# Kernel tuning notes

Measured on AMD Instinct MI355X. Metric: run time of the kernel, lower is better.

## Reference

```python
import jax, jax.numpy as jnp
import numpy as np

N = 100000      # nodes
E = 1600000     # edges (avg degree 16)
F_IN = 128      # num_features
H = 64          # num_hidden
C = 40          # num_classes


def setup_inputs() -> dict:
    key = jax.random.key(0)
    ks = jax.random.split(key, 12)
    glorot = lambda k, fi, fo: jax.random.normal(k, (fi, fo), jnp.float32) * np.float32(1.0 / np.sqrt(fi))
    return {
        "x": jax.random.normal(ks[0], (N, F_IN), jnp.float32),
        "edge_index": jax.random.randint(ks[1], (2, E), 0, N, jnp.int64),
        "conv0_w": glorot(ks[2], F_IN, H), "conv0_b": jnp.zeros((H,), jnp.float32),
        "lin0_w": glorot(ks[3], H, H),     "lin0_b": jnp.zeros((H,), jnp.float32),
        "conv1_w": glorot(ks[4], H, H),    "conv1_b": jnp.zeros((H,), jnp.float32),
        "lin1_w": glorot(ks[5], H, H),     "lin1_b": jnp.zeros((H,), jnp.float32),
        "out_w": glorot(ks[6], 2 * H, C),  "out_b": jnp.zeros((C,), jnp.float32),
    }


def _gcn_conv(h, W, b, src, dst, norm, n):
    # h: [N, din] -> transform then symmetric-normalized scatter-add aggregation
    m = (h @ W)[src] * norm[:, None]           # [E+N, dout] gathered messages
    return jax.ops.segment_sum(m, dst, num_segments=n) + b


def reference(x, edge_index, conv0_w, conv0_b, lin0_w, lin0_b,
              conv1_w, conv1_b, lin1_w, lin1_b, out_w, out_b):
    n = x.shape[0]
    loops = jnp.arange(n, dtype=edge_index.dtype)
    src = jnp.concatenate([edge_index[0], loops])  # self-loops appended (GCNConv default)
    dst = jnp.concatenate([edge_index[1], loops])
    deg = jax.ops.segment_sum(jnp.ones_like(dst, x.dtype), dst, num_segments=n)
    dinv = jnp.where(deg > 0, jax.lax.rsqrt(deg), 0.0)
    norm = dinv[src] * dinv[dst]                   # D^-1/2 A D^-1/2 edge weights

    # layer 0 (dropout omitted: eval mode for deterministic reference)
    h = jax.nn.elu(_gcn_conv(x, conv0_w, conv0_b, src, dst, norm, n))
    y0 = h @ lin0_w + lin0_b
    # layer 1
    h = jax.nn.elu(_gcn_conv(h, conv1_w, conv1_b, src, dst, norm, n))
    y1 = h @ lin1_w + lin1_b

    z = jnp.concatenate([y0, y1], axis=1)          # [N, 2H] jumping-knowledge concat
    return z @ out_w + out_b                       # [N, C]
```

## Files before the change

kernel.cpp:

```cpp
#include <hip/hip_runtime.h>

#define DEVFN __device__ __forceinline__

typedef __attribute__((ext_vector_type(8))) short short8;
typedef __attribute__((ext_vector_type(4))) float float4v;

DEVFN float bf2f(unsigned short u) {
    union { unsigned int i; float f; } c;
    c.i = ((unsigned int)u) << 16;
    return c.f;
}

DEVFN unsigned short f2bf(float f) {
    union { float f; unsigned int i; } c;
    c.f = f;
    unsigned int u = c.i;
    return (unsigned short)((u + 0x7FFFu + ((u >> 16) & 1u)) >> 16);
}

DEVFN void addu4(float* acc, uint4 u) {
    unsigned int w[4] = {u.x, u.y, u.z, u.w};
#pragma unroll
    for (int k = 0; k < 4; k++) {
        union { unsigned int i; float f; } lo, hi;
        lo.i = w[k] << 16;
        hi.i = w[k] & 0xFFFF0000u;
        acc[2 * k]     += lo.f;
        acc[2 * k + 1] += hi.f;
    }
}


#define CHUNK 4096

__global__ __launch_bounds__(256) void k_count(const int* __restrict__ dst,
                                               int* __restrict__ Cmat, int E) {
    __shared__ int lh[1024];
    int t = threadIdx.x;
    for (int b = t; b < 1024; b += 256) lh[b] = 0;
    __syncthreads();
    int i0 = blockIdx.x * CHUNK;
    int i1 = i0 + CHUNK; if (i1 > E) i1 = E;
    for (int i = i0 + t; i < i1; i += 256) atomicAdd(&lh[dst[i] >> 8], 1);
    __syncthreads();
    int* row = Cmat + (size_t)blockIdx.x * 1024;
    for (int b = t; b < 1024; b += 256) row[b] = lh[b];
}

__global__ __launch_bounds__(256) void k_wscan(const int* __restrict__ Cmat,
                                               int* __restrict__ Omat,
                                               int* __restrict__ btot, int gC) {
    int b = (blockIdx.x * 256 + threadIdx.x) >> 6;
    int lane = threadIdx.x & 63;
    int base = 0;
    for (int c0 = 0; c0 < gC; c0 += 64) {
        int c = c0 + lane;
        int x = (c < gC) ? Cmat[(size_t)c * 1024 + b] : 0;
        int orig = x;
#pragma unroll
        for (int off = 1; off < 64; off <<= 1) {
            int y = __shfl_up(x, off);
            if (lane >= off) x += y;
        }
        if (c < gC) Omat[(size_t)c * 1024 + b] = base + x - orig;
        base += __shfl(x, 63);
    }
    if (lane == 0) btot[b] = base;
}

__global__ __launch_bounds__(1024) void k_bscan(const int* __restrict__ btot,
                                                int* __restrict__ boff) {
    __shared__ int s[1024];
    int t = threadIdx.x;
    int v = btot[t];
    s[t] = v;
    __syncthreads();
    for (int o = 1; o < 1024; o <<= 1) {
        int x = (t >= o) ? s[t - o] : 0;
        __syncthreads();
        s[t] += x;
        __syncthreads();
    }
    boff[t] = s[t] - v;
    if (t == 1023) boff[1024] = s[t];
}

__global__ __launch_bounds__(256) void k_part2(const int* __restrict__ src,
                                               const int* __restrict__ dst,
                                               const int* __restrict__ Omat,
                                               const int* __restrict__ boff,
                                               unsigned int* __restrict__ part, int E) {
    __shared__ int lb[1024];
    __shared__ int lc[1024];
    int t = threadIdx.x;
    const int* orow = Omat + (size_t)blockIdx.x * 1024;
    for (int b = t; b < 1024; b += 256) {
        lb[b] = boff[b] + orow[b];
        lc[b] = 0;
    }
    __syncthreads();
    int i0 = blockIdx.x * CHUNK;
    int i1 = i0 + CHUNK; if (i1 > E) i1 = E;
    for (int i = i0 + t; i < i1; i += 256) {
        int d = dst[i];
        int b = d >> 8;
        int r = atomicAdd(&lc[b], 1);
        part[lb[b] + r] = (unsigned int)src[i] | ((unsigned int)(d & 255) << 24);
    }
}

__global__ __launch_bounds__(256) void k_fill_local(const unsigned int* __restrict__ part,
                                                    const int* __restrict__ boff,
                                                    float* __restrict__ dinv,
                                                    int* __restrict__ roff,
                                                    int* __restrict__ csr, int n) {
    __shared__ int lcnt[256];
    __shared__ int lsc[256];
    __shared__ int lcur[256];
    int b = blockIdx.x, t = threadIdx.x;
    int s0 = boff[b], s1 = boff[b + 1];
    lcnt[t] = 0;
    __syncthreads();
    for (int i = s0 + t; i < s1; i += 256) atomicAdd(&lcnt[part[i] >> 24], 1);
    __syncthreads();
    int v = lcnt[t];
    lsc[t] = v;
    __syncthreads();
    for (int o = 1; o < 256; o <<= 1) {
        int x = (t >= o) ? lsc[t - o] : 0;
        __syncthreads();
        lsc[t] += x;
        __syncthreads();
    }
    int excl = lsc[t] - v;
    int node = (b << 8) + t;
    if (node < n) {
        dinv[node] = rsqrtf((float)(v + 1));
        roff[node] = s0 + excl + v;
    }
    lcur[t] = s0 + excl;
    __syncthreads();
    for (int i = s0 + t; i < s1; i += 256) {
        unsigned int p = part[i];
        int pos = atomicAdd(&lcur[p >> 24], 1);
        csr[pos] = (int)(p & 0xFFFFFFu);
    }
}

__global__ void k_fuse(const float* __restrict__ lin0_w, const float* __restrict__ lin0_b,
                       const float* __restrict__ lin1_w, const float* __restrict__ lin1_b,
                       const float* __restrict__ out_w, const float* __restrict__ out_b,
                       float* __restrict__ Wf0, float* __restrict__ Wf1, float* __restrict__ bf) {
    int idx = blockIdx.x * blockDim.x + threadIdx.x;
    if (idx < 2560) {
        int i = idx / 40, j = idx % 40;
        float a = 0.f;
        for (int k = 0; k < 64; k++) a += lin0_w[i * 64 + k] * out_w[k * 40 + j];
        Wf0[idx] = a;
    } else if (idx < 5120) {
        int r = idx - 2560;
        int i = r / 40, j = r % 40;
        float a = 0.f;
        for (int k = 0; k < 64; k++) a += lin1_w[i * 64 + k] * out_w[(64 + k) * 40 + j];
        Wf1[r] = a;
    } else if (idx < 5160) {
        int j = idx - 5120;
        float a = out_b[j];
        for (int k = 0; k < 64; k++) {
            a += lin0_b[k] * out_w[k * 40 + j];
            a += lin1_b[k] * out_w[(64 + k) * 40 + j];
        }
        bf[j] = a;
    }
}

__global__ __launch_bounds__(256) void k_prepw(const float* __restrict__ W0,
                                               const float* __restrict__ W1,
                                               const float* __restrict__ Wf0,
                                               const float* __restrict__ Wf1,
                                               unsigned short* __restrict__ Wb0,
                                               unsigned short* __restrict__ Wb1,
                                               unsigned short* __restrict__ Wfb0,
                                               unsigned short* __restrict__ Wfb1) {
    int tid = blockIdx.x * 256 + threadIdx.x;
    if (tid < 1024) {
        int ks = tid >> 8, rem = tid & 255;
        int nt = rem >> 6, lane = rem & 63;
        int quad = lane >> 4, c = lane & 15;
        union { unsigned short h[8]; uint4 u; } p;
#pragma unroll
        for (int j = 0; j < 8; j++)
            p.h[j] = f2bf(W0[(ks * 32 + quad * 8 + j) * 64 + nt * 16 + c]);
        *(uint4*)(Wb0 + (size_t)tid * 8) = p.u;
    } else if (tid < 1536) {
        int t2 = tid - 1024;
        int ks = t2 >> 8, rem = t2 & 255;
        int nt = rem >> 6, lane = rem & 63;
        int quad = lane >> 4, c = lane & 15;
        union { unsigned short h[8]; uint4 u; } p;
#pragma unroll
        for (int j = 0; j < 8; j++)
            p.h[j] = f2bf(W1[(ks * 32 + quad * 8 + j) * 64 + nt * 16 + c]);
        *(uint4*)(Wb1 + (size_t)t2 * 8) = p.u;
    } else if (tid < 1920) {
        int t2 = tid - 1536;
        int ks = t2 / 192;
        int rem = t2 % 192;
        int nt = rem >> 6, lane = rem & 63;
        int quad = lane >> 4, c = lane & 15;
        int col = nt * 16 + c;
        union { unsigned short h[8]; uint4 u; } p;
#pragma unroll
        for (int j = 0; j < 8; j++)
            p.h[j] = (col < 40) ? f2bf(Wf0[(ks * 32 + quad * 8 + j) * 40 + col]) : (unsigned short)0;
        *(uint4*)(Wfb0 + ((size_t)(ks * 3 + nt) * 64 + lane) * 8) = p.u;
    } else if (tid < 2304) {
        int t2 = tid - 1920;
        int ks = t2 / 192;
        int rem = t2 % 192;
        int nt = rem >> 6, lane = rem & 63;
        int quad = lane >> 4, c = lane & 15;
        int col = nt * 16 + c;
        union { unsigned short h[8]; uint4 u; } p;
#pragma unroll
        for (int j = 0; j < 8; j++)
            p.h[j] = (col < 40) ? f2bf(Wf1[(ks * 32 + quad * 8 + j) * 40 + col]) : (unsigned short)0;
        *(uint4*)(Wfb1 + ((size_t)(ks * 3 + nt) * 64 + lane) * 8) = p.u;
    }
}


__global__ __launch_bounds__(256) void k_gemm_128(const float* __restrict__ A,
                                                  const unsigned short* __restrict__ Wb,
                                                  const float* __restrict__ dinv,
                                                  unsigned short* __restrict__ Cb, int n) {
    __shared__ unsigned short aLDS[64 * 144];
    int t = threadIdx.x;
    int r0 = blockIdx.x * 64;
    for (int idx = t; idx < 2048; idx += 256) {
        int r = idx >> 5;
        int k = (idx & 31) << 2;
        int gr = r0 + r; if (gr >= n) gr = n - 1;
        float4 u = *(const float4*)(A + (size_t)gr * 128 + k);
        int tile = r >> 4, m = r & 15;
        int ks = k >> 5, quad = (k >> 3) & 3, j0 = k & 7;
        int g = (tile * 4 + ks) * 4 + quad;
        union { unsigned short h[4]; uint2 u2; } pk;
        pk.h[0] = f2bf(u.x); pk.h[1] = f2bf(u.y); pk.h[2] = f2bf(u.z); pk.h[3] = f2bf(u.w);
        *(uint2*)(aLDS + g * 144 + m * 8 + j0) = pk.u2;
    }
    int lane = t & 63;
    int w = t >> 6;
    short8 bfr[4][4];
#pragma unroll
    for (int ks = 0; ks < 4; ks++)
#pragma unroll
        for (int nt = 0; nt < 4; nt++)
            bfr[ks][nt] = *(const short8*)(Wb + ((size_t)(ks * 4 + nt) * 64 + lane) * 8);
    __syncthreads();
    int quad = lane >> 4, m = lane & 15;
    short8 afr[4];
#pragma unroll
    for (int ks = 0; ks < 4; ks++)
        afr[ks] = *(const short8*)(aLDS + ((w * 4 + ks) * 4 + quad) * 144 + m * 8);
    float4v acc[4] = {};
#pragma unroll
    for (int nt = 0; nt < 4; nt++)
#pragma unroll
        for (int ks = 0; ks < 4; ks++)
            acc[nt] = __builtin_amdgcn_mfma_f32_16x16x32_bf16(afr[ks], bfr[ks][nt], acc[nt], 0, 0, 0);
    float dv[4];
#pragma unroll
    for (int reg = 0; reg < 4; reg++) {
        int gr = r0 + w * 16 + quad * 4 + reg;
        dv[reg] = (gr < n) ? dinv[gr] : 0.f;
    }
#pragma unroll
    for (int nt = 0; nt < 4; nt++)
#pragma unroll
        for (int reg = 0; reg < 4; reg++) {
            int gr = r0 + w * 16 + quad * 4 + reg;
            if (gr < n) Cb[(size_t)gr * 64 + nt * 16 + m] = f2bf(dv[reg] * acc[nt][reg]);
        }
}

__global__ __launch_bounds__(256) void k_gemm_64(const unsigned short* __restrict__ A,
                                                 const unsigned short* __restrict__ Wb,
                                                 const float* __restrict__ dinv,
                                                 unsigned short* __restrict__ Cb, int n) {
    __shared__ unsigned short aLDS[32 * 144];
    int t = threadIdx.x;
    int r0 = blockIdx.x * 64;
    for (int idx = t; idx < 512; idx += 256) {
        int r = idx >> 3, j = idx & 7;
        int gr = r0 + r; if (gr >= n) gr = n - 1;
        uint4 u = *(const uint4*)(A + (size_t)gr * 64 + j * 8);
        int tile = r >> 4, m = r & 15;
        int ks = j >> 2, quad = j & 3;
        *(uint4*)(aLDS + ((tile * 2 + ks) * 4 + quad) * 144 + m * 8) = u;
    }
    int lane = t & 63;
    int w = t >> 6;
    short8 bfr[2][4];
#pragma unroll
    for (int ks = 0; ks < 2; ks++)
#pragma unroll
        for (int nt = 0; nt < 4; nt++)
            bfr[ks][nt] = *(const short8*)(Wb + ((size_t)(ks * 4 + nt) * 64 + lane) * 8);
    __syncthreads();
    int quad = lane >> 4, m = lane & 15;
    short8 afr[2];
#pragma unroll
    for (int ks = 0; ks < 2; ks++)
        afr[ks] = *(const short8*)(aLDS + ((w * 2 + ks) * 4 + quad) * 144 + m * 8);
    float4v acc[4] = {};
#pragma unroll
    for (int nt = 0; nt < 4; nt++)
#pragma unroll
        for (int ks = 0; ks < 2; ks++)
            acc[nt] = __builtin_amdgcn_mfma_f32_16x16x32_bf16(afr[ks], bfr[ks][nt], acc[nt], 0, 0, 0);
    float dv[4];
#pragma unroll
    for (int reg = 0; reg < 4; reg++) {
        int gr = r0 + w * 16 + quad * 4 + reg;
        dv[reg] = (gr < n) ? dinv[gr] : 0.f;
    }
#pragma unroll
    for (int nt = 0; nt < 4; nt++)
#pragma unroll
        for (int reg = 0; reg < 4; reg++) {
            int gr = r0 + w * 16 + quad * 4 + reg;
            if (gr < n) Cb[(size_t)gr * 64 + nt * 16 + m] = f2bf(dv[reg] * acc[nt][reg]);
        }
}

__global__ __launch_bounds__(256) void k_head(const unsigned short* __restrict__ Hb,
                                              const unsigned short* __restrict__ Wfb,
                                              const float* __restrict__ bfv,
                                              float* __restrict__ O, int n, int add) {
    __shared__ unsigned short aLDS[32 * 144];
    int t = threadIdx.x;
    int r0 = blockIdx.x * 64;
    for (int idx = t; idx < 512; idx += 256) {
        int r = idx >> 3, j = idx & 7;
        int gr = r0 + r; if (gr >= n) gr = n - 1;
        uint4 u = *(const uint4*)(Hb + (size_t)gr * 64 + j * 8);
        int tile = r >> 4, m = r & 15;
        int ks = j >> 2, quad = j & 3;
        *(uint4*)(aLDS + ((tile * 2 + ks) * 4 + quad) * 144 + m * 8) = u;
    }
    int lane = t & 63;
    int w = t >> 6;
    short8 bfr[2][3];
#pragma unroll
    for (int ks = 0; ks < 2; ks++)
#pragma unroll
        for (int nt = 0; nt < 3; nt++)
            bfr[ks][nt] = *(const short8*)(Wfb + ((size_t)(ks * 3 + nt) * 64 + lane) * 8);
    __syncthreads();
    int quad = lane >> 4, m = lane & 15;
    short8 afr[2];
#pragma unroll
    for (int ks = 0; ks < 2; ks++)
        afr[ks] = *(const short8*)(aLDS + ((w * 2 + ks) * 4 + quad) * 144 + m * 8);
    float4v acc[3] = {};
#pragma unroll
    for (int nt = 0; nt < 3; nt++)
#pragma unroll
        for (int ks = 0; ks < 2; ks++)
            acc[nt] = __builtin_amdgcn_mfma_f32_16x16x32_bf16(afr[ks], bfr[ks][nt], acc[nt], 0, 0, 0);
#pragma unroll
    for (int nt = 0; nt < 3; nt++) {
        int col = nt * 16 + m;
        if (col < 40) {
            float bb = add ? bfv[col] : 0.f;
#pragma unroll
            for (int reg = 0; reg < 4; reg++) {
                int gr = r0 + w * 16 + quad * 4 + reg;
                if (gr < n) {
                    size_t p = (size_t)gr * 40 + col;
                    if (add) O[p] = O[p] + acc[nt][reg] + bb;
                    else     O[p] = acc[nt][reg];
                }
            }
        }
    }
}

__global__ __launch_bounds__(256) void k_agg(const unsigned short* __restrict__ T,
                                             const int* __restrict__ csr,
                                             const int* __restrict__ roffE,
                                             const float* __restrict__ bias,
                                             unsigned short* __restrict__ Hb, int n) {
    int lane = threadIdx.x & 63;
    int q = lane >> 3, h = lane & 7;
    int v = blockIdx.x * 4 + (threadIdx.x >> 6);
    if (v >= n) return;
    int start = (v == 0) ? 0 : roffE[v - 1];
    int end = roffE[v];
    float dv = rsqrtf((float)(end - start + 1));
    float acc[8] = {0.f, 0.f, 0.f, 0.f, 0.f, 0.f, 0.f, 0.f};
    if (q == 0) {
        uint4 u = *(const uint4*)(T + (size_t)v * 64 + h * 8);
        addu4(acc, u);
    }
    for (int base = start; base < end; base += 64) {
        int m = end - base; if (m > 64) m = 64;
        int e = (lane < m) ? csr[base + lane] : 0;
        int j = 0;
        for (; j + 32 <= m; j += 32) {
            int s0 = __shfl(e, j + q);
            int s1 = __shfl(e, j + 8 + q);
            int s2 = __shfl(e, j + 16 + q);
            int s3 = __shfl(e, j + 24 + q);
            uint4 u0 = *(const uint4*)(T + (size_t)s0 * 64 + h * 8);
            uint4 u1 = *(const uint4*)(T + (size_t)s1 * 64 + h * 8);
            uint4 u2 = *(const uint4*)(T + (size_t)s2 * 64 + h * 8);
            uint4 u3 = *(const uint4*)(T + (size_t)s3 * 64 + h * 8);
            addu4(acc, u0); addu4(acc, u1); addu4(acc, u2); addu4(acc, u3);
        }
        if (j + 16 <= m) {
            int s0 = __shfl(e, j + q);
            int s1 = __shfl(e, j + 8 + q);
            uint4 u0 = *(const uint4*)(T + (size_t)s0 * 64 + h * 8);
            uint4 u1 = *(const uint4*)(T + (size_t)s1 * 64 + h * 8);
            addu4(acc, u0); addu4(acc, u1);
            j += 16;
        }
        if (j + 8 <= m) {
            int s = __shfl(e, j + q);
            uint4 u = *(const uint4*)(T + (size_t)s * 64 + h * 8);
            addu4(acc, u);
            j += 8;
        }
        if (j < m) {
            int jj = j + q;
            int s = __shfl(e, jj & 63);
            if (jj < m) {
                uint4 u = *(const uint4*)(T + (size_t)s * 64 + h * 8);
                addu4(acc, u);
            }
        }
    }
#pragma unroll
    for (int i = 0; i < 8; i++) {
        acc[i] += __shfl_xor(acc[i], 8);
        acc[i] += __shfl_xor(acc[i], 16);
        acc[i] += __shfl_xor(acc[i], 32);
    }
    if (q == 0) {
        float4 b0 = *(const float4*)(bias + h * 8);
        float4 b1 = *(const float4*)(bias + h * 8 + 4);
        float bb[8] = {b0.x, b0.y, b0.z, b0.w, b1.x, b1.y, b1.z, b1.w};
        union { unsigned short hh[8]; uint4 u; } p;
#pragma unroll
        for (int i = 0; i < 8; i++) {
            float r = dv * acc[i] + bb[i];
            r = (r > 0.f) ? r : (__expf(r) - 1.f);
            p.hh[i] = f2bf(r);
        }
        *(uint4*)(Hb + (size_t)v * 64 + h * 8) = p.u;
    }
}


extern "C" void kernel_launch(void* const* d_in, const int* in_sizes, int n_in,
                              void* d_out, int out_size, void* d_ws, size_t ws_size,
                              hipStream_t stream) {
    const float* x       = (const float*)d_in[0];
    const int*   eidx    = (const int*)d_in[1];
    const float* conv0_w = (const float*)d_in[2];
    const float* conv0_b = (const float*)d_in[3];
    const float* lin0_w  = (const float*)d_in[4];
    const float* lin0_b  = (const float*)d_in[5];
    const float* conv1_w = (const float*)d_in[6];
    const float* conv1_b = (const float*)d_in[7];
    const float* lin1_w  = (const float*)d_in[8];
    const float* lin1_b  = (const float*)d_in[9];
    const float* out_w   = (const float*)d_in[10];
    const float* out_b   = (const float*)d_in[11];

    int n = in_sizes[0] / 128;
    int E = in_sizes[1] / 2;
    const int* src = eidx;
    const int* dst = eidx + E;
    int NB = (n + 255) >> 8;
    int gC = (E + CHUNK - 1) / CHUNK;

    char* wsb = (char*)d_ws;
    auto al = [](size_t v) { return (v + 4095) & ~(size_t)4095; };
    size_t o = 0;
    int*            Cmat  = (int*)(wsb + o);            o = al(o + (size_t)gC * 1024 * 4);
    int*            Omat  = (int*)(wsb + o);            o = al(o + (size_t)gC * 1024 * 4);
    int*            btot  = (int*)(wsb + o);            o = al(o + 1024 * 4);
    int*            boff  = (int*)(wsb + o);            o = al(o + 1025 * 4);
    float*          dinv  = (float*)(wsb + o);          o = al(o + (size_t)n * 4);
    int*            roff  = (int*)(wsb + o);            o = al(o + (size_t)n * 4);
    unsigned int*   part  = (unsigned int*)(wsb + o);   o = al(o + (size_t)E * 4);
    int*            csr   = (int*)(wsb + o);            o = al(o + (size_t)E * 4);
    float*          Wf0   = (float*)(wsb + o);          o = al(o + 2560 * 4);
    float*          Wf1   = (float*)(wsb + o);          o = al(o + 2560 * 4);
    float*          bfv   = (float*)(wsb + o);          o = al(o + 40 * 4);
    unsigned short* Wb0   = (unsigned short*)(wsb + o); o = al(o + 8192 * 2);
    unsigned short* Wb1   = (unsigned short*)(wsb + o); o = al(o + 4096 * 2);
    unsigned short* Wfb0  = (unsigned short*)(wsb + o); o = al(o + 3072 * 2);
    unsigned short* Wfb1  = (unsigned short*)(wsb + o); o = al(o + 3072 * 2);
    unsigned short* Ab    = (unsigned short*)(wsb + o); o = al(o + (size_t)n * 64 * 2);
    unsigned short* Hb    = (unsigned short*)(wsb + o); o = al(o + (size_t)n * 64 * 2);
    float* O = (float*)d_out;

    int gT = (n + 63) / 64;
    int gV = (n + 3) / 4;

    k_count<<<gC, 256, 0, stream>>>(dst, Cmat, E);
    k_wscan<<<256, 256, 0, stream>>>(Cmat, Omat, btot, gC);
    k_bscan<<<1, 1024, 0, stream>>>(btot, boff);
    k_part2<<<gC, 256, 0, stream>>>(src, dst, Omat, boff, part, E);
    k_fill_local<<<NB, 256, 0, stream>>>(part, boff, dinv, roff, csr, n);
    k_fuse<<<(5160 + 255) / 256, 256, 0, stream>>>(lin0_w, lin0_b, lin1_w, lin1_b, out_w, out_b,
                                                   Wf0, Wf1, bfv);
    k_prepw<<<9, 256, 0, stream>>>(conv0_w, conv1_w, Wf0, Wf1, Wb0, Wb1, Wfb0, Wfb1);

    k_gemm_128<<<gT, 256, 0, stream>>>(x, Wb0, dinv, Ab, n);
    k_agg<<<gV, 256, 0, stream>>>(Ab, csr, roff, conv0_b, Hb, n);
    k_head<<<gT, 256, 0, stream>>>(Hb, Wfb0, bfv, O, n, 0);
    k_gemm_64<<<gT, 256, 0, stream>>>(Hb, Wb1, dinv, Ab, n);
    k_agg<<<gV, 256, 0, stream>>>(Ab, csr, roff, conv1_b, Hb, n);
    k_head<<<gT, 256, 0, stream>>>(Hb, Wfb1, bfv, O, n, 1);
}
```

Baseline: 297.8 us.

## Fuse layer-1 GEMM with head-0, merge weight prep, half-wave per node in aggregation

Merges the k_fuse and k_prepw weight-preparation kernels into one k_prep launch that computes the folded head weights directly. Fuses the first head projection with the second-layer GEMM into k_mid, so H is read once for both. Changes the aggregation kernel to process two nodes per wavefront using 32-lane halves, which cuts idle lanes for average degree 16 and removes one shuffle reduction step. Together these reduce launch count and memory traffic, at the cost of more register pressure in the fused kernel and less per-node parallelism for high-degree nodes.

```diff
diff --git a/kernel.cpp b/kernel.cpp
--- a/kernel.cpp
+++ b/kernel.cpp
@@ -147,41 +147,16 @@
     }
 }
 
-__global__ void k_fuse(const float* __restrict__ lin0_w, const float* __restrict__ lin0_b,
-                       const float* __restrict__ lin1_w, const float* __restrict__ lin1_b,
-                       const float* __restrict__ out_w, const float* __restrict__ out_b,
-                       float* __restrict__ Wf0, float* __restrict__ Wf1, float* __restrict__ bf) {
-    int idx = blockIdx.x * blockDim.x + threadIdx.x;
-    if (idx < 2560) {
-        int i = idx / 40, j = idx % 40;
-        float a = 0.f;
-        for (int k = 0; k < 64; k++) a += lin0_w[i * 64 + k] * out_w[k * 40 + j];
-        Wf0[idx] = a;
-    } else if (idx < 5120) {
-        int r = idx - 2560;
-        int i = r / 40, j = r % 40;
-        float a = 0.f;
-        for (int k = 0; k < 64; k++) a += lin1_w[i * 64 + k] * out_w[(64 + k) * 40 + j];
-        Wf1[r] = a;
-    } else if (idx < 5160) {
-        int j = idx - 5120;
-        float a = out_b[j];
-        for (int k = 0; k < 64; k++) {
-            a += lin0_b[k] * out_w[k * 40 + j];
-            a += lin1_b[k] * out_w[(64 + k) * 40 + j];
-        }
-        bf[j] = a;
-    }
-}
-
-__global__ __launch_bounds__(256) void k_prepw(const float* __restrict__ W0,
-                                               const float* __restrict__ W1,
-                                               const float* __restrict__ Wf0,
-                                               const float* __restrict__ Wf1,
-                                               unsigned short* __restrict__ Wb0,
-                                               unsigned short* __restrict__ Wb1,
-                                               unsigned short* __restrict__ Wfb0,
-                                               unsigned short* __restrict__ Wfb1) {
+__global__ __launch_bounds__(256) void k_prep(const float* __restrict__ W0,
+                                              const float* __restrict__ W1,
+                                              const float* __restrict__ lin0_w, const float* __restrict__ lin0_b,
+                                              const float* __restrict__ lin1_w, const float* __restrict__ lin1_b,
+                                              const float* __restrict__ out_w, const float* __restrict__ out_b,
+                                              unsigned short* __restrict__ Wb0,
+                                              unsigned short* __restrict__ Wb1,
+                                              unsigned short* __restrict__ Wfb0,
+                                              unsigned short* __restrict__ Wfb1,
+                                              float* __restrict__ bfv) {
     int tid = blockIdx.x * 256 + threadIdx.x;
     if (tid < 1024) {
         int ks = tid >> 8, rem = tid & 255;
@@ -211,8 +186,16 @@
         int col = nt * 16 + c;
         union { unsigned short h[8]; uint4 u; } p;
 #pragma unroll
-        for (int j = 0; j < 8; j++)
-            p.h[j] = (col < 40) ? f2bf(Wf0[(ks * 32 + quad * 8 + j) * 40 + col]) : (unsigned short)0;
+        for (int j = 0; j < 8; j++) {
+            unsigned short r = 0;
+            if (col < 40) {
+                int i = ks * 32 + quad * 8 + j;
+                float a = 0.f;
+                for (int k = 0; k < 64; k++) a += lin0_w[i * 64 + k] * out_w[k * 40 + col];
+                r = f2bf(a);
+            }
+            p.h[j] = r;
+        }
         *(uint4*)(Wfb0 + ((size_t)(ks * 3 + nt) * 64 + lane) * 8) = p.u;
     } else if (tid < 2304) {
         int t2 = tid - 1920;
@@ -223,9 +206,25 @@
         int col = nt * 16 + c;
         union { unsigned short h[8]; uint4 u; } p;
 #pragma unroll
-        for (int j = 0; j < 8; j++)
-            p.h[j] = (col < 40) ? f2bf(Wf1[(ks * 32 + quad * 8 + j) * 40 + col]) : (unsigned short)0;
+        for (int j = 0; j < 8; j++) {
+            unsigned short r = 0;
+            if (col < 40) {
+                int i = ks * 32 + quad * 8 + j;
+                float a = 0.f;
+                for (int k = 0; k < 64; k++) a += lin1_w[i * 64 + k] * out_w[(64 + k) * 40 + col];
+                r = f2bf(a);
+            }
+            p.h[j] = r;
+        }
         *(uint4*)(Wfb1 + ((size_t)(ks * 3 + nt) * 64 + lane) * 8) = p.u;
+    } else if (tid < 2344) {
+        int j = tid - 2304;
+        float a = out_b[j];
+        for (int k = 0; k < 64; k++) {
+            a += lin0_b[k] * out_w[k * 40 + j];
+            a += lin1_b[k] * out_w[(64 + k) * 40 + j];
+        }
+        bfv[j] = a;
     }
 }
 
@@ -284,60 +283,12 @@
         }
 }
 
-__global__ __launch_bounds__(256) void k_gemm_64(const unsigned short* __restrict__ A,
-                                                 const unsigned short* __restrict__ Wb,
-                                                 const float* __restrict__ dinv,
-                                                 unsigned short* __restrict__ Cb, int n) {
-    __shared__ unsigned short aLDS[32 * 144];
-    int t = threadIdx.x;
-    int r0 = blockIdx.x * 64;
-    for (int idx = t; idx < 512; idx += 256) {
-        int r = idx >> 3, j = idx & 7;
-        int gr = r0 + r; if (gr >= n) gr = n - 1;
-        uint4 u = *(const uint4*)(A + (size_t)gr * 64 + j * 8);
-        int tile = r >> 4, m = r & 15;
-        int ks = j >> 2, quad = j & 3;
-        *(uint4*)(aLDS + ((tile * 2 + ks) * 4 + quad) * 144 + m * 8) = u;
-    }
-    int lane = t & 63;
-    int w = t >> 6;
-    short8 bfr[2][4];
-#pragma unroll
-    for (int ks = 0; ks < 2; ks++)
-#pragma unroll
-        for (int nt = 0; nt < 4; nt++)
-            bfr[ks][nt] = *(const short8*)(Wb + ((size_t)(ks * 4 + nt) * 64 + lane) * 8);
-    __syncthreads();
-    int quad = lane >> 4, m = lane & 15;
-    short8 afr[2];
-#pragma unroll
-    for (int ks = 0; ks < 2; ks++)
-        afr[ks] = *(const short8*)(aLDS + ((w * 2 + ks) * 4 + quad) * 144 + m * 8);
-    float4v acc[4] = {};
-#pragma unroll
-    for (int nt = 0; nt < 4; nt++)
-#pragma unroll
-        for (int ks = 0; ks < 2; ks++)
-            acc[nt] = __builtin_amdgcn_mfma_f32_16x16x32_bf16(afr[ks], bfr[ks][nt], acc[nt], 0, 0, 0);
-    float dv[4];
-#pragma unroll
-    for (int reg = 0; reg < 4; reg++) {
-        int gr = r0 + w * 16 + quad * 4 + reg;
-        dv[reg] = (gr < n) ? dinv[gr] : 0.f;
-    }
-#pragma unroll
-    for (int nt = 0; nt < 4; nt++)
-#pragma unroll
-        for (int reg = 0; reg < 4; reg++) {
-            int gr = r0 + w * 16 + quad * 4 + reg;
-            if (gr < n) Cb[(size_t)gr * 64 + nt * 16 + m] = f2bf(dv[reg] * acc[nt][reg]);
-        }
-}
-
-__global__ __launch_bounds__(256) void k_head(const unsigned short* __restrict__ Hb,
-                                              const unsigned short* __restrict__ Wfb,
-                                              const float* __restrict__ bfv,
-                                              float* __restrict__ O, int n, int add) {
+__global__ __launch_bounds__(256) void k_mid(const unsigned short* __restrict__ Hb,
+                                             const unsigned short* __restrict__ Wb,
+                                             const unsigned short* __restrict__ Wfb,
+                                             const float* __restrict__ dinv,
+                                             unsigned short* __restrict__ Ab,
+                                             float* __restrict__ O, int n) {
     __shared__ unsigned short aLDS[32 * 144];
     int t = threadIdx.x;
     int r0 = blockIdx.x * 64;
@@ -351,6 +302,77 @@
     }
     int lane = t & 63;
     int w = t >> 6;
+    short8 bG[2][4], bH[2][3];
+#pragma unroll
+    for (int ks = 0; ks < 2; ks++) {
+#pragma unroll
+        for (int nt = 0; nt < 4; nt++)
+            bG[ks][nt] = *(const short8*)(Wb + ((size_t)(ks * 4 + nt) * 64 + lane) * 8);
+#pragma unroll
+        for (int nt = 0; nt < 3; nt++)
+            bH[ks][nt] = *(const short8*)(Wfb + ((size_t)(ks * 3 + nt) * 64 + lane) * 8);
+    }
+    __syncthreads();
+    int quad = lane >> 4, m = lane & 15;
+    short8 afr[2];
+#pragma unroll
+    for (int ks = 0; ks < 2; ks++)
+        afr[ks] = *(const short8*)(aLDS + ((w * 2 + ks) * 4 + quad) * 144 + m * 8);
+    float4v accG[4] = {};
+    float4v accH[3] = {};
+#pragma unroll
+    for (int nt = 0; nt < 4; nt++)
+#pragma unroll
+        for (int ks = 0; ks < 2; ks++)
+            accG[nt] = __builtin_amdgcn_mfma_f32_16x16x32_bf16(afr[ks], bG[ks][nt], accG[nt], 0, 0, 0);
+#pragma unroll
+    for (int nt = 0; nt < 3; nt++)
+#pragma unroll
+        for (int ks = 0; ks < 2; ks++)
+            accH[nt] = __builtin_amdgcn_mfma_f32_16x16x32_bf16(afr[ks], bH[ks][nt], accH[nt], 0, 0, 0);
+    float dv[4];
+#pragma unroll
+    for (int reg = 0; reg < 4; reg++) {
+        int gr = r0 + w * 16 + quad * 4 + reg;
+        dv[reg] = (gr < n) ? dinv[gr] : 0.f;
+    }
+#pragma unroll
+    for (int nt = 0; nt < 4; nt++)
+#pragma unroll
+        for (int reg = 0; reg < 4; reg++) {
+            int gr = r0 + w * 16 + quad * 4 + reg;
+            if (gr < n) Ab[(size_t)gr * 64 + nt * 16 + m] = f2bf(dv[reg] * accG[nt][reg]);
+        }
+#pragma unroll
+    for (int nt = 0; nt < 3; nt++) {
+        int col = nt * 16 + m;
+        if (col < 40) {
+#pragma unroll
+            for (int reg = 0; reg < 4; reg++) {
+                int gr = r0 + w * 16 + quad * 4 + reg;
+                if (gr < n) O[(size_t)gr * 40 + col] = accH[nt][reg];
+            }
+        }
+    }
+}
+
+__global__ __launch_bounds__(256) void k_head(const unsigned short* __restrict__ Hb,
+                                              const unsigned short* __restrict__ Wfb,
+                                              const float* __restrict__ bfv,
+                                              float* __restrict__ O, int n) {
+    __shared__ unsigned short aLDS[32 * 144];
+    int t = threadIdx.x;
+    int r0 = blockIdx.x * 64;
+    for (int idx = t; idx < 512; idx += 256) {
+        int r = idx >> 3, j = idx & 7;
+        int gr = r0 + r; if (gr >= n) gr = n - 1;
+        uint4 u = *(const uint4*)(Hb + (size_t)gr * 64 + j * 8);
+        int tile = r >> 4, m = r & 15;
+        int ks = j >> 2, quad = j & 3;
+        *(uint4*)(aLDS + ((tile * 2 + ks) * 4 + quad) * 144 + m * 8) = u;
+    }
+    int lane = t & 63;
+    int w = t >> 6;
     short8 bfr[2][3];
 #pragma unroll
     for (int ks = 0; ks < 2; ks++)
@@ -373,14 +395,13 @@
     for (int nt = 0; nt < 3; nt++) {
         int col = nt * 16 + m;
         if (col < 40) {
-            float bb = add ? bfv[col] : 0.f;
+            float bb = bfv[col];
 #pragma unroll
             for (int reg = 0; reg < 4; reg++) {
                 int gr = r0 + w * 16 + quad * 4 + reg;
                 if (gr < n) {
                     size_t p = (size_t)gr * 40 + col;
-                    if (add) O[p] = O[p] + acc[nt][reg] + bb;
-                    else     O[p] = acc[nt][reg];
+                    O[p] = O[p] + acc[nt][reg] + bb;
                 }
             }
         }
@@ -393,8 +414,11 @@
                                              const float* __restrict__ bias,
                                              unsigned short* __restrict__ Hb, int n) {
     int lane = threadIdx.x & 63;
-    int q = lane >> 3, h = lane & 7;
-    int v = blockIdx.x * 4 + (threadIdx.x >> 6);
+    int half = lane >> 5;
+    int sub = lane & 31;
+    int q = sub >> 3, h = sub & 7;
+    int hb = half << 5;
+    int v = blockIdx.x * 8 + ((threadIdx.x >> 6) << 1) + half;
     if (v >= n) return;
     int start = (v == 0) ? 0 : roffE[v - 1];
     int end = roffE[v];
@@ -404,38 +428,38 @@
         uint4 u = *(const uint4*)(T + (size_t)v * 64 + h * 8);
         addu4(acc, u);
     }
-    for (int base = start; base < end; base += 64) {
-        int m = end - base; if (m > 64) m = 64;
-        int e = (lane < m) ? csr[base + lane] : 0;
+    for (int base = start; base < end; base += 32) {
+        int m = end - base; if (m > 32) m = 32;
+        int e = (sub < m) ? csr[base + sub] : 0;
         int j = 0;
-        for (; j + 32 <= m; j += 32) {
-            int s0 = __shfl(e, j + q);
-            int s1 = __shfl(e, j + 8 + q);
-            int s2 = __shfl(e, j + 16 + q);
-            int s3 = __shfl(e, j + 24 + q);
+        for (; j + 16 <= m; j += 16) {
+            int s0 = __shfl(e, hb + j + q);
+            int s1 = __shfl(e, hb + j + 4 + q);
+            int s2 = __shfl(e, hb + j + 8 + q);
+            int s3 = __shfl(e, hb + j + 12 + q);
             uint4 u0 = *(const uint4*)(T + (size_t)s0 * 64 + h * 8);
             uint4 u1 = *(const uint4*)(T + (size_t)s1 * 64 + h * 8);
             uint4 u2 = *(const uint4*)(T + (size_t)s2 * 64 + h * 8);
             uint4 u3 = *(const uint4*)(T + (size_t)s3 * 64 + h * 8);
             addu4(acc, u0); addu4(acc, u1); addu4(acc, u2); addu4(acc, u3);
         }
-        if (j + 16 <= m) {
-            int s0 = __shfl(e, j + q);
-            int s1 = __shfl(e, j + 8 + q);
+        if (j + 8 <= m) {
+            int s0 = __shfl(e, hb + j + q);
+            int s1 = __shfl(e, hb + j + 4 + q);
             uint4 u0 = *(const uint4*)(T + (size_t)s0 * 64 + h * 8);
             uint4 u1 = *(const uint4*)(T + (size_t)s1 * 64 + h * 8);
             addu4(acc, u0); addu4(acc, u1);
-            j += 16;
-        }
-        if (j + 8 <= m) {
-            int s = __shfl(e, j + q);
+            j += 8;
+        }
+        if (j + 4 <= m) {
+            int s = __shfl(e, hb + j + q);
             uint4 u = *(const uint4*)(T + (size_t)s * 64 + h * 8);
             addu4(acc, u);
-            j += 8;
+            j += 4;
         }
         if (j < m) {
             int jj = j + q;
-            int s = __shfl(e, jj & 63);
+            int s = __shfl(e, hb + (jj & 31));
             if (jj < m) {
                 uint4 u = *(const uint4*)(T + (size_t)s * 64 + h * 8);
                 addu4(acc, u);
@@ -446,7 +470,6 @@
     for (int i = 0; i < 8; i++) {
         acc[i] += __shfl_xor(acc[i], 8);
         acc[i] += __shfl_xor(acc[i], 16);
-        acc[i] += __shfl_xor(acc[i], 32);
     }
     if (q == 0) {
         float4 b0 = *(const float4*)(bias + h * 8);
@@ -498,8 +521,6 @@
     int*            roff  = (int*)(wsb + o);            o = al(o + (size_t)n * 4);
     unsigned int*   part  = (unsigned int*)(wsb + o);   o = al(o + (size_t)E * 4);
     int*            csr   = (int*)(wsb + o);            o = al(o + (size_t)E * 4);
-    float*          Wf0   = (float*)(wsb + o);          o = al(o + 2560 * 4);
-    float*          Wf1   = (float*)(wsb + o);          o = al(o + 2560 * 4);
     float*          bfv   = (float*)(wsb + o);          o = al(o + 40 * 4);
     unsigned short* Wb0   = (unsigned short*)(wsb + o); o = al(o + 8192 * 2);
     unsigned short* Wb1   = (unsigned short*)(wsb + o); o = al(o + 4096 * 2);
@@ -510,21 +531,19 @@
     float* O = (float*)d_out;
 
     int gT = (n + 63) / 64;
-    int gV = (n + 3) / 4;
+    int gV = (n + 7) / 8;
 
     k_count<<<gC, 256, 0, stream>>>(dst, Cmat, E);
     k_wscan<<<256, 256, 0, stream>>>(Cmat, Omat, btot, gC);
     k_bscan<<<1, 1024, 0, stream>>>(btot, boff);
     k_part2<<<gC, 256, 0, stream>>>(src, dst, Omat, boff, part, E);
     k_fill_local<<<NB, 256, 0, stream>>>(part, boff, dinv, roff, csr, n);
-    k_fuse<<<(5160 + 255) / 256, 256, 0, stream>>>(lin0_w, lin0_b, lin1_w, lin1_b, out_w, out_b,
-                                                   Wf0, Wf1, bfv);
-    k_prepw<<<9, 256, 0, stream>>>(conv0_w, conv1_w, Wf0, Wf1, Wb0, Wb1, Wfb0, Wfb1);
+    k_prep<<<10, 256, 0, stream>>>(conv0_w, conv1_w, lin0_w, lin0_b, lin1_w, lin1_b,
+                                   out_w, out_b, Wb0, Wb1, Wfb0, Wfb1, bfv);
 
     k_gemm_128<<<gT, 256, 0, stream>>>(x, Wb0, dinv, Ab, n);
     k_agg<<<gV, 256, 0, stream>>>(Ab, csr, roff, conv0_b, Hb, n);
-    k_head<<<gT, 256, 0, stream>>>(Hb, Wfb0, bfv, O, n, 0);
-    k_gemm_64<<<gT, 256, 0, stream>>>(Hb, Wb1, dinv, Ab, n);
+    k_mid<<<gT, 256, 0, stream>>>(Hb, Wb1, Wfb0, dinv, Ab, O, n);
     k_agg<<<gV, 256, 0, stream>>>(Ab, csr, roff, conv1_b, Hb, n);
-    k_head<<<gT, 256, 0, stream>>>(Hb, Wfb1, bfv, O, n, 1);
-}
+    k_head<<<gT, 256, 0, stream>>>(Hb, Wfb1, bfv, O, n);
+}
```

Measured after the change: 275.6 us. 7.5% less time.
